# Performance work log

Hardware: AMD Instinct MI355X
Metric: run time of the kernel (lower is better)

The kernel has to match this reference:

```python
import jax, jax.numpy as jnp
import numpy as np

B, C, N = 2, 29, 8192
S, K = 1024, 16  # npoint, nsample
D = C + 3


def fps(xyz_t, npoint):
    # xyz_t: [B, N, 3] -> indices [B, npoint] (furthest point sampling, starts at idx 0)
    b, n, _ = xyz_t.shape

    def step(carry, _):
        dists, farthest = carry  # [B,N], [B]
        centroid = jnp.take_along_axis(xyz_t, farthest[:, None, None], axis=1)  # [B,1,3]
        d = jnp.sum((xyz_t - centroid) ** 2, axis=-1)  # [B,N]
        dists = jnp.minimum(dists, d)
        nxt = jnp.argmax(dists, axis=-1)
        return (dists, nxt), farthest

    init = (jnp.full((b, n), 1e10, xyz_t.dtype), jnp.zeros((b,), jnp.int32))
    _, idx = jax.lax.scan(step, init, None, length=npoint)
    return jnp.transpose(idx)  # [B, npoint]


def knn_self(pts, k):
    # pts: [B, S, 3] -> k nearest neighbor indices within the same set, [B, S, k]
    sq = jnp.sum(pts * pts, axis=-1)
    d2 = sq[:, :, None] + sq[:, None, :] - 2.0 * jnp.einsum('bic,bjc->bij', pts, pts)
    _, idx = jax.lax.top_k(-d2, k)
    return idx


def group(arr, idx):
    # arr: [B, C, N], idx: [B, S, K] -> [B, C, S, K]
    return jax.vmap(lambda a, i: a[:, i])(arr, idx)


def squeeze_2x2(x):
    # RealNVP alt-order squeeze: [n, c, h, w] -> [n, 4c, h/2, w/2]
    tl = x[:, :, 0::2, 0::2]
    br = x[:, :, 1::2, 1::2]
    tr = x[:, :, 0::2, 1::2]
    bl = x[:, :, 1::2, 0::2]
    return jnp.concatenate([tl, br, tr, bl], axis=1)


def conv2d(x, w):
    return jax.lax.conv_general_dilated(
        x, w, window_strides=(1, 1), padding='VALID',
        dimension_numbers=('NCHW', 'OIHW', 'NCHW'))


def setup_inputs() -> dict:
    key = jax.random.key(0)
    ks = jax.random.split(key, 6)
    return {
        'xyz': jax.random.normal(ks[0], (B, 3, N), jnp.float32),
        'feats': jax.random.normal(ks[1], (B, C, N), jnp.float32),
        'w0': jax.random.normal(ks[2], (64, 2 * D * 4, 3, 3), jnp.float32) * 0.02,
        'w1': jax.random.normal(ks[3], (64, 64, 3, 3), jnp.float32) * 0.02,
        'w2': jax.random.normal(ks[4], (128, 64, 3, 3), jnp.float32) * 0.02,
        'w3': jax.random.normal(ks[5], (128, 128, 2, 2), jnp.float32) * 0.02,
    }


def reference(xyz, feats, w0, w1, w2, w3):
    b, c, n = feats.shape
    xyz_t = jnp.transpose(xyz, (0, 2, 1))  # [B,N,3]
    fps_idx = fps(xyz_t, S)  # [B,S]
    new_xyz = jnp.take_along_axis(xyz, fps_idx[:, None, :], axis=2)  # [B,3,S]
    new_xyz_t = jnp.transpose(new_xyz, (0, 2, 1))  # [B,S,3]
    idx = knn_self(new_xyz_t, K)  # [B,S,K], values in [0,S)

    pos_grouped = group(new_xyz, idx)  # [B,3,S,K]
    feats_grouped = group(feats, idx)  # [B,C,S,K] (indices < S, as in original)
    pos_diff = pos_grouped - new_xyz[:, :, :, None]
    fg = jnp.concatenate([pos_diff, feats_grouped], axis=1)  # [B,D,S,K]

    # pairwise outer-product features; second half ([fg;1] x [fg;1] upper block) is all ones
    outer = jnp.einsum('bdsi,bdsj->bdsij', fg, fg)  # [B,D,S,K,K]
    mat = jnp.concatenate([outer, jnp.ones_like(outer)], axis=1)  # [B,2D,S,K,K]
    mat = jnp.transpose(mat, (0, 2, 1, 3, 4)).reshape(b * S, 2 * D, K, K)
    mat = squeeze_2x2(mat)  # [B*S, 8D, K/2, K/2]

    for w in (w0, w1, w2, w3):  # use_bn=False -> Identity bns; spatial 8->6->4->2->1
        mat = jax.nn.relu(conv2d(mat, w))

    new_points = jnp.transpose(mat.reshape(b, S, -1), (0, 2, 1))  # [B,128,S]
    return new_xyz, new_points, fps_idx
```

## Files before the change

kernel.cpp:

```cpp
#include <hip/hip_runtime.h>
#include <hip/hip_bf16.h>

#pragma clang fp contract(off)

#define NPTS 8192
#define NS   1024
#define NB   2
#define NC   29
#define NK   16


__global__ __launch_bounds__(256) void prep_kernel(
    const float* __restrict__ w0, const float* __restrict__ w1,
    const float* __restrict__ w2, const float* __restrict__ w3,
    float* __restrict__ w0t, float* __restrict__ w1t,
    float* __restrict__ w2t, float* __restrict__ w3t,
    float* __restrict__ bias0)
{
    int i = blockIdx.x * 256 + threadIdx.x;
    int n = gridDim.x * 256;
    for (int e = i; e < 73728; e += n) {
        int o = e & 63, r = e >> 6, tap = r % 9, ic2 = r / 9;
        int ic = ((ic2 >> 5) << 6) + (ic2 & 31);
        w0t[e] = w0[(o * 256 + ic) * 9 + tap];
    }
    for (int e = i; e < 36864; e += n) {
        int o = e & 63, r = e >> 6, tap = r % 9, ic = r / 9;
        w1t[e] = w1[(o * 64 + ic) * 9 + tap];
    }
    for (int e = i; e < 73728; e += n) {
        int o = e & 127, r = e >> 7, tap = r % 9, ic = r / 9;
        w2t[e] = w2[(o * 64 + ic) * 9 + tap];
    }
    for (int e = i; e < 65536; e += n) {
        int o = e & 127, r = e >> 7, tap = r & 3, ic = r >> 2;
        w3t[e] = w3[(o * 128 + ic) * 4 + tap];
    }
    if (i < 64) {
        float sum = 0.0f;
        for (int q = 0; q < 4; ++q)
            for (int c = 0; c < 32; ++c)
                for (int t = 0; t < 9; ++t)
                    sum += w0[(i * 256 + q * 64 + 32 + c) * 9 + t];
        bias0[i] = sum;
    }
}

__device__ __forceinline__ float wave_max_nonneg(float x) {
    int v = __float_as_int(x);
    int t;
    t = __builtin_amdgcn_update_dpp(0, v, 0x111, 0xf, 0xf, true);
    v = __float_as_int(fmaxf(__int_as_float(v), __int_as_float(t)));
    t = __builtin_amdgcn_update_dpp(0, v, 0x112, 0xf, 0xf, true);
    v = __float_as_int(fmaxf(__int_as_float(v), __int_as_float(t)));
    t = __builtin_amdgcn_update_dpp(0, v, 0x114, 0xf, 0xf, true);
    v = __float_as_int(fmaxf(__int_as_float(v), __int_as_float(t)));
    t = __builtin_amdgcn_update_dpp(0, v, 0x118, 0xf, 0xf, true);
    v = __float_as_int(fmaxf(__int_as_float(v), __int_as_float(t)));
    t = __builtin_amdgcn_update_dpp(0, v, 0x142, 0xa, 0xf, true);
    v = __float_as_int(fmaxf(__int_as_float(v), __int_as_float(t)));
    t = __builtin_amdgcn_update_dpp(0, v, 0x143, 0xc, 0xf, true);
    v = __float_as_int(fmaxf(__int_as_float(v), __int_as_float(t)));
    return __int_as_float(__builtin_amdgcn_readlane(v, 63));
}

__global__ __launch_bounds__(512, 2) void fps_kernel(
    const float* __restrict__ xyz,
    float* __restrict__ nx_ws, float* __restrict__ out)
{
    int b = blockIdx.x;
    int tid = threadIdx.x;
    const float* X = xyz + b * 3 * NPTS;

    __shared__ float s_xyz[3 * NPTS];
    __shared__ unsigned long long s_key[NS];

    float px[16], py[16], pz[16], dist[16];
#pragma unroll
    for (int i = 0; i < 16; ++i) {
        int gi = i * 512 + tid;
        float x = X[gi], y = X[NPTS + gi], z = X[2 * NPTS + gi];
        px[i] = x; py[i] = y; pz[i] = z;
        dist[i] = 1e10f;
        s_xyz[gi] = x; s_xyz[NPTS + gi] = y; s_xyz[2 * NPTS + gi] = z;
    }
    for (int i = tid; i < NS; i += 512) s_key[i] = 0ull;
    if (tid == 0) s_key[0] = 0xFFFFFFFFull;
    __syncthreads();

    float cx = s_xyz[0], cy = s_xyz[NPTS], cz = s_xyz[2 * NPTS];

    for (int it = 1; it < NS; ++it) {
#pragma unroll
        for (int i = 0; i < 16; ++i)
            asm volatile("" : "+v"(px[i]), "+v"(py[i]), "+v"(pz[i]));
#pragma unroll
        for (int i = 0; i < 16; ++i) {
            float dx = px[i] - cx, dy = py[i] - cy, dz = pz[i] - cz;
            float d = (dx * dx + dy * dy) + dz * dz;
            dist[i] = fminf(dist[i], d);
        }
        float t8[8];
#pragma unroll
        for (int i = 0; i < 8; ++i) t8[i] = fmaxf(dist[2 * i], dist[2 * i + 1]);
        float t4[4];
#pragma unroll
        for (int i = 0; i < 4; ++i) t4[i] = fmaxf(t8[2 * i], t8[2 * i + 1]);
        float bv = fmaxf(fmaxf(t4[0], t4[1]), fmaxf(t4[2], t4[3]));
        float wm = wave_max_nonneg(bv);
        if (bv == wm) {
            int gi = 0;
#pragma unroll
            for (int i = 15; i >= 0; --i)
                if (dist[i] == wm) gi = i * 512 + tid;
            unsigned long long key =
                ((unsigned long long)__float_as_uint(wm) << 32) | (unsigned)(~gi);
            atomicMax(&s_key[it], key);
        }
        __syncthreads();
        int idx = (int)(~(unsigned)s_key[it]);
        cx = s_xyz[idx]; cy = s_xyz[NPTS + idx]; cz = s_xyz[2 * NPTS + idx];
    }

    float* out_fps = out + 268288 + b * NS;
    for (int i = tid; i < NS; i += 512) {
        int j = (int)(~(unsigned)s_key[i]);
        out_fps[i] = (float)j;
        float x = s_xyz[j], y = s_xyz[NPTS + j], z = s_xyz[2 * NPTS + j];
        nx_ws[(b * 3 + 0) * NS + i] = x; out[(b * 3 + 0) * NS + i] = x;
        nx_ws[(b * 3 + 1) * NS + i] = y; out[(b * 3 + 1) * NS + i] = y;
        nx_ws[(b * 3 + 2) * NS + i] = z; out[(b * 3 + 2) * NS + i] = z;
    }
}

__global__ __launch_bounds__(256) void knn_kernel(
    const float* __restrict__ nx_ws, int* __restrict__ knn_ws)
{
    int q = blockIdx.x * 4 + (threadIdx.x >> 6);
    int lane = threadIdx.x & 63;
    int b = q >> 10, s = q & 1023;
    const float* P = nx_ws + b * 3 * NS;
    float qx = P[s], qy = P[NS + s], qz = P[2 * NS + s];
    float sqq = (qx * qx + qy * qy) + qz * qz;
    int base_j = lane * 16;
    float d2[16];
    {
        const float4* x4 = (const float4*)(P + base_j);
        const float4* y4 = (const float4*)(P + NS + base_j);
        const float4* z4 = (const float4*)(P + 2 * NS + base_j);
#pragma unroll
        for (int t = 0; t < 4; ++t) {
            float4 xv = x4[t], yv = y4[t], zv = z4[t];
            float xs[4] = { xv.x, xv.y, xv.z, xv.w };
            float ys[4] = { yv.x, yv.y, yv.z, yv.w };
            float zs[4] = { zv.x, zv.y, zv.z, zv.w };
#pragma unroll
            for (int e = 0; e < 4; ++e) {
                float xj = xs[e], yj = ys[e], zj = zs[e];
                float sqj = (xj * xj + yj * yj) + zj * zj;
                float dot = (qx * xj + qy * yj) + qz * zj;
                d2[t * 4 + e] = (sqq + sqj) - 2.0f * dot;
            }
        }
    }
    for (int r = 0; r < NK; ++r) {
        float lv = 3.0e38f; int li = 0;
#pragma unroll
        for (int i = 0; i < 16; ++i) { if (d2[i] < lv) { lv = d2[i]; li = i; } }
        int gj = base_j + li;
#pragma unroll
        for (int off = 32; off > 0; off >>= 1) {
            float ov = __shfl_xor(lv, off, 64);
            int   oj = __shfl_xor(gj, off, 64);
            if (ov < lv || (ov == lv && oj < gj)) { lv = ov; gj = oj; }
        }
        if (lane == 0) knn_ws[q * NK + r] = gj;
        if ((gj >> 4) == lane) {
            int li2 = gj & 15;
#pragma unroll
            for (int i = 0; i < 16; ++i) if (i == li2) d2[i] = 3.0e38f;
        }
    }
}

template<int G>
__device__ __forceinline__ void conv0_accum(
    const float* __restrict__ s_fg, const float* __restrict__ wbase, float acc[9])
{
    constexpr int r0 = G + (G >> 1);
    constexpr int GODD = G & 1;
#pragma unroll
    for (int q = 0; q < 4; ++q) {
        const int ro = q & 1, co = ((q + 1) >> 1) & 1;
        const float* wq = wbase + q * 32 * 9 * 64;
        for (int ch = 0; ch < 32; ++ch) {
            const float4* f4 = (const float4*)(s_fg + ch * 16);
            float4 v0 = f4[0], v1 = f4[1], v2 = f4[2], v3 = f4[3];
            float fg[16] = { v0.x, v0.y, v0.z, v0.w,  v1.x, v1.y, v1.z, v1.w,
                             v2.x, v2.y, v2.z, v2.w,  v3.x, v3.y, v3.z, v3.w };
            float rr[32];
#pragma unroll
            for (int j = 0; j < 4; ++j) {
                float aj = fg[2 * (r0 + j) + ro];
#pragma unroll
                for (int v = 0; v < 8; ++v)
                    rr[j * 8 + v] = aj * fg[2 * v + co];
            }
            float w[9];
#pragma unroll
            for (int t = 0; t < 9; ++t) w[t] = wq[(ch * 9 + t) * 64];
#pragma unroll
            for (int pp = 0; pp < 9; ++pp) {
                const int ly = GODD ? (pp < 3 ? 0 : 1) : (pp < 6 ? 0 : 1);
                const int xx = GODD ? (pp < 3 ? pp + 3 : pp - 3) : (pp < 6 ? pp : pp - 6);
#pragma unroll
                for (int ky = 0; ky < 3; ++ky)
#pragma unroll
                    for (int kx = 0; kx < 3; ++kx)
                        acc[pp] = __builtin_fmaf(w[ky * 3 + kx], rr[(ly + ky) * 8 + xx + kx], acc[pp]);
            }
        }
    }
}

__global__ __launch_bounds__(256, 4) void conv_kernel(
    const float* __restrict__ feats, const float* __restrict__ nx_ws,
    const int* __restrict__ knn_ws,
    const float* __restrict__ w0t, const float* __restrict__ bias0,
    const float* __restrict__ w1t, const float* __restrict__ w2t,
    const float* __restrict__ w3t, float* __restrict__ out)
{
    __shared__ float s_fg[512];
    __shared__ int   s_ni[16];
    __shared__ float s_a1[64 * 36];
    __shared__ float s_a2[64 * 16];
    __shared__ float s_a3[128 * 4];

    int bs = blockIdx.x, b = bs >> 10, s = bs & 1023;
    int tid = threadIdx.x;
    if (tid < 16) s_ni[tid] = knn_ws[bs * NK + tid];
    __syncthreads();
    const float* P = nx_ws + b * 3 * NS;
#pragma unroll
    for (int e = tid; e < 512; e += 256) {
        int d = e >> 4, k = e & 15; int j = s_ni[k];
        float v = (d < 3) ? (P[d * NS + j] - P[d * NS + s])
                          : feats[(b * NC + (d - 3)) * NPTS + j];
        s_fg[e] = v;
    }
    __syncthreads();

    int o = tid & 63, g = tid >> 6;
    {
        float acc[9];
        float bz = bias0[o];
#pragma unroll
        for (int p = 0; p < 9; ++p) acc[p] = bz;
        const float* wb = w0t + o;
        if      (g == 0) conv0_accum<0>(s_fg, wb, acc);
        else if (g == 1) conv0_accum<1>(s_fg, wb, acc);
        else if (g == 2) conv0_accum<2>(s_fg, wb, acc);
        else             conv0_accum<3>(s_fg, wb, acc);
#pragma unroll
        for (int pp = 0; pp < 9; ++pp) s_a1[o * 36 + g * 9 + pp] = fmaxf(acc[pp], 0.0f);
    }
    __syncthreads();
    {
        float a[4] = {0, 0, 0, 0};
        const float* wb = w1t + o;
        for (int ic = 0; ic < 64; ++ic) {
            const float2* ar2 = (const float2*)(s_a1 + ic * 36 + g * 6);
            float r[18];
#pragma unroll
            for (int t = 0; t < 9; ++t) { float2 tv = ar2[t]; r[t*2] = tv.x; r[t*2+1] = tv.y; }
            float w[9];
#pragma unroll
            for (int t = 0; t < 9; ++t) w[t] = wb[(ic * 9 + t) * 64];
#pragma unroll
            for (int x = 0; x < 4; ++x)
#pragma unroll
                for (int ky = 0; ky < 3; ++ky)
#pragma unroll
                    for (int kx = 0; kx < 3; ++kx)
                        a[x] = __builtin_fmaf(w[ky * 3 + kx], r[ky * 6 + x + kx], a[x]);
        }
#pragma unroll
        for (int x = 0; x < 4; ++x) s_a2[o * 16 + g * 4 + x] = fmaxf(a[x], 0.0f);
    }
    __syncthreads();
    {
        int o2 = tid & 127, g2 = tid >> 7;
        float a[2] = {0, 0};
        const float* wb = w2t + o2;
        for (int ic = 0; ic < 64; ++ic) {
            const float4* ar4 = (const float4*)(s_a2 + ic * 16 + g2 * 4);
            float r[12];
#pragma unroll
            for (int t = 0; t < 3; ++t) { float4 tv = ar4[t]; r[t*4]=tv.x; r[t*4+1]=tv.y; r[t*4+2]=tv.z; r[t*4+3]=tv.w; }
            float w[9];
#pragma unroll
            for (int t = 0; t < 9; ++t) w[t] = wb[(ic * 9 + t) * 128];
#pragma unroll
            for (int x = 0; x < 2; ++x)
#pragma unroll
                for (int ky = 0; ky < 3; ++ky)
#pragma unroll
                    for (int kx = 0; kx < 3; ++kx)
                        a[x] = __builtin_fmaf(w[ky * 3 + kx], r[ky * 4 + x + kx], a[x]);
        }
#pragma unroll
        for (int x = 0; x < 2; ++x) s_a3[o2 * 4 + g2 * 2 + x] = fmaxf(a[x], 0.0f);
    }
    __syncthreads();
    if (tid < 128) {
        float acc = 0.0f;
        const float* wb = w3t + tid;
        for (int ic = 0; ic < 128; ++ic) {
            float4 av = *(const float4*)(s_a3 + ic * 4);
            float wa = wb[(ic * 4 + 0) * 128];
            float wbv = wb[(ic * 4 + 1) * 128];
            float wc = wb[(ic * 4 + 2) * 128];
            float wd = wb[(ic * 4 + 3) * 128];
            acc = __builtin_fmaf(wa, av.x, acc);
            acc = __builtin_fmaf(wbv, av.y, acc);
            acc = __builtin_fmaf(wc, av.z, acc);
            acc = __builtin_fmaf(wd, av.w, acc);
        }
        out[6144 + (b * 128 + tid) * NS + s] = fmaxf(acc, 0.0f);
    }
}

extern "C" void kernel_launch(void* const* d_in, const int* in_sizes, int n_in,
                              void* d_out, int out_size, void* d_ws, size_t ws_size,
                              hipStream_t stream) {
    const float* xyz   = (const float*)d_in[0];
    const float* feats = (const float*)d_in[1];
    const float* w0    = (const float*)d_in[2];
    const float* w1    = (const float*)d_in[3];
    const float* w2    = (const float*)d_in[4];
    const float* w3    = (const float*)d_in[5];
    float* out = (float*)d_out;

    char* ws = (char*)d_ws;
    float* nx_ws  = (float*)(ws + 8192);
    int*   knn_ws = (int*)(ws + 32768);
    float* w0t    = (float*)(ws + 163840);
    float* bias0  = (float*)(ws + 458752);
    float* w1t    = (float*)(ws + 459008);
    float* w2t    = (float*)(ws + 606464);
    float* w3t    = (float*)(ws + 901376);

    prep_kernel<<<128, 256, 0, stream>>>(w0, w1, w2, w3, w0t, w1t, w2t, w3t, bias0);
    fps_kernel<<<NB, 512, 0, stream>>>(xyz, nx_ws, out);
    knn_kernel<<<(NB * NS) / 4, 256, 0, stream>>>(nx_ws, knn_ws);
    conv_kernel<<<NB * NS, 256, 0, stream>>>(feats, nx_ws, knn_ws, w0t, bias0, w1t, w2t, w3t, out);
}
```

Before: 1.431 ms.

## Stage conv0 and conv1 weights through double-buffered shared memory

Conv0 and conv1 now load their weights from global memory cooperatively, four input channels at a time, into a double-buffered shared-memory tile. The next chunk is prefetched into registers while the current chunk is consumed. Previously each of the four thread groups fetched the same weights from global memory on its own. This aims to cut redundant global/L1 traffic and hide load latency, at the cost of about 18KB more LDS per block and a barrier per chunk, including barriers inside branches that differ per group.

```diff
diff --git a/kernel.cpp b/kernel.cpp
--- a/kernel.cpp
+++ b/kernel.cpp
@@ -184,41 +184,69 @@
 }
 
 template<int G>
-__device__ __forceinline__ void conv0_accum(
-    const float* __restrict__ s_fg, const float* __restrict__ wbase, float acc[9])
+__device__ __forceinline__ void conv0_staged(
+    const float* __restrict__ s_fg, float* __restrict__ s_w,
+    const float* __restrict__ w0t, int o, float acc[9])
 {
     constexpr int r0 = G + (G >> 1);
     constexpr int GODD = G & 1;
+    {
+        float st[9];
+#pragma unroll
+        for (int j = 0; j < 9; ++j) st[j] = w0t[(G * 9 + j) * 64 + o];
+#pragma unroll
+        for (int j = 0; j < 9; ++j) s_w[(G * 9 + j) * 64 + o] = st[j];
+    }
+    __syncthreads();
+    int buf = 0;
 #pragma unroll
     for (int q = 0; q < 4; ++q) {
         const int ro = q & 1, co = ((q + 1) >> 1) & 1;
-        const float* wq = wbase + q * 32 * 9 * 64;
-        for (int ch = 0; ch < 32; ++ch) {
-            const float4* f4 = (const float4*)(s_fg + ch * 16);
-            float4 v0 = f4[0], v1 = f4[1], v2 = f4[2], v3 = f4[3];
-            float fg[16] = { v0.x, v0.y, v0.z, v0.w,  v1.x, v1.y, v1.z, v1.w,
-                             v2.x, v2.y, v2.z, v2.w,  v3.x, v3.y, v3.z, v3.w };
-            float rr[32];
-#pragma unroll
-            for (int j = 0; j < 4; ++j) {
-                float aj = fg[2 * (r0 + j) + ro];
-#pragma unroll
-                for (int v = 0; v < 8; ++v)
-                    rr[j * 8 + v] = aj * fg[2 * v + co];
-            }
-            float w[9];
-#pragma unroll
-            for (int t = 0; t < 9; ++t) w[t] = wq[(ch * 9 + t) * 64];
-#pragma unroll
-            for (int pp = 0; pp < 9; ++pp) {
-                const int ly = GODD ? (pp < 3 ? 0 : 1) : (pp < 6 ? 0 : 1);
-                const int xx = GODD ? (pp < 3 ? pp + 3 : pp - 3) : (pp < 6 ? pp : pp - 6);
-#pragma unroll
-                for (int ky = 0; ky < 3; ++ky)
-#pragma unroll
-                    for (int kx = 0; kx < 3; ++kx)
-                        acc[pp] = __builtin_fmaf(w[ky * 3 + kx], rr[(ly + ky) * 8 + xx + kx], acc[pp]);
-            }
+        for (int cc = 0; cc < 8; ++cc) {
+            int K = q * 8 + cc;
+            float st[9];
+            if (K < 31) {
+                const float* gsrc = w0t + (K + 1) * 36 * 64;
+#pragma unroll
+                for (int j = 0; j < 9; ++j) st[j] = gsrc[(G * 9 + j) * 64 + o];
+            }
+            const float* wl = s_w + buf * 2304;
+#pragma unroll
+            for (int chl = 0; chl < 4; ++chl) {
+                int ch = cc * 4 + chl;
+                const float4* f4 = (const float4*)(s_fg + ch * 16);
+                float4 v0 = f4[0], v1 = f4[1], v2 = f4[2], v3 = f4[3];
+                float fg[16] = { v0.x, v0.y, v0.z, v0.w,  v1.x, v1.y, v1.z, v1.w,
+                                 v2.x, v2.y, v2.z, v2.w,  v3.x, v3.y, v3.z, v3.w };
+                float rr[32];
+#pragma unroll
+                for (int j = 0; j < 4; ++j) {
+                    float aj = fg[2 * (r0 + j) + ro];
+#pragma unroll
+                    for (int v = 0; v < 8; ++v)
+                        rr[j * 8 + v] = aj * fg[2 * v + co];
+                }
+                float w[9];
+#pragma unroll
+                for (int t = 0; t < 9; ++t) w[t] = wl[(chl * 9 + t) * 64 + o];
+#pragma unroll
+                for (int pp = 0; pp < 9; ++pp) {
+                    const int ly = GODD ? (pp < 3 ? 0 : 1) : (pp < 6 ? 0 : 1);
+                    const int xx = GODD ? (pp < 3 ? pp + 3 : pp - 3) : (pp < 6 ? pp : pp - 6);
+#pragma unroll
+                    for (int ky = 0; ky < 3; ++ky)
+#pragma unroll
+                        for (int kx = 0; kx < 3; ++kx)
+                            acc[pp] = __builtin_fmaf(w[ky * 3 + kx], rr[(ly + ky) * 8 + xx + kx], acc[pp]);
+                }
+            }
+            if (K < 31) {
+                float* wn = s_w + (buf ^ 1) * 2304;
+#pragma unroll
+                for (int j = 0; j < 9; ++j) wn[(G * 9 + j) * 64 + o] = st[j];
+            }
+            __syncthreads();
+            buf ^= 1;
         }
     }
 }
@@ -232,6 +260,7 @@
 {
     __shared__ float s_fg[512];
     __shared__ int   s_ni[16];
+    __shared__ float s_w[2 * 36 * 64];
     __shared__ float s_a1[64 * 36];
     __shared__ float s_a2[64 * 16];
     __shared__ float s_a3[128 * 4];
@@ -256,33 +285,57 @@
         float bz = bias0[o];
 #pragma unroll
         for (int p = 0; p < 9; ++p) acc[p] = bz;
-        const float* wb = w0t + o;
-        if      (g == 0) conv0_accum<0>(s_fg, wb, acc);
-        else if (g == 1) conv0_accum<1>(s_fg, wb, acc);
-        else if (g == 2) conv0_accum<2>(s_fg, wb, acc);
-        else             conv0_accum<3>(s_fg, wb, acc);
+        if      (g == 0) conv0_staged<0>(s_fg, s_w, w0t, o, acc);
+        else if (g == 1) conv0_staged<1>(s_fg, s_w, w0t, o, acc);
+        else if (g == 2) conv0_staged<2>(s_fg, s_w, w0t, o, acc);
+        else             conv0_staged<3>(s_fg, s_w, w0t, o, acc);
 #pragma unroll
         for (int pp = 0; pp < 9; ++pp) s_a1[o * 36 + g * 9 + pp] = fmaxf(acc[pp], 0.0f);
     }
+    {
+        float st[9];
+#pragma unroll
+        for (int j = 0; j < 9; ++j) st[j] = w1t[(g * 9 + j) * 64 + o];
+#pragma unroll
+        for (int j = 0; j < 9; ++j) s_w[(g * 9 + j) * 64 + o] = st[j];
+    }
     __syncthreads();
     {
         float a[4] = {0, 0, 0, 0};
-        const float* wb = w1t + o;
-        for (int ic = 0; ic < 64; ++ic) {
-            const float2* ar2 = (const float2*)(s_a1 + ic * 36 + g * 6);
-            float r[18];
-#pragma unroll
-            for (int t = 0; t < 9; ++t) { float2 tv = ar2[t]; r[t*2] = tv.x; r[t*2+1] = tv.y; }
-            float w[9];
-#pragma unroll
-            for (int t = 0; t < 9; ++t) w[t] = wb[(ic * 9 + t) * 64];
-#pragma unroll
-            for (int x = 0; x < 4; ++x)
-#pragma unroll
-                for (int ky = 0; ky < 3; ++ky)
-#pragma unroll
-                    for (int kx = 0; kx < 3; ++kx)
-                        a[x] = __builtin_fmaf(w[ky * 3 + kx], r[ky * 6 + x + kx], a[x]);
+        int buf = 0;
+        for (int c = 0; c < 16; ++c) {
+            float st[9];
+            if (c < 15) {
+                const float* gsrc = w1t + (c + 1) * 36 * 64;
+#pragma unroll
+                for (int j = 0; j < 9; ++j) st[j] = gsrc[(g * 9 + j) * 64 + o];
+            }
+            const float* wl = s_w + buf * 2304;
+#pragma unroll
+            for (int icl = 0; icl < 4; ++icl) {
+                int ic = c * 4 + icl;
+                const float2* ar2 = (const float2*)(s_a1 + ic * 36 + g * 6);
+                float r[18];
+#pragma unroll
+                for (int t = 0; t < 9; ++t) { float2 tv = ar2[t]; r[t*2] = tv.x; r[t*2+1] = tv.y; }
+                float w[9];
+#pragma unroll
+                for (int t = 0; t < 9; ++t) w[t] = wl[(icl * 9 + t) * 64 + o];
+#pragma unroll
+                for (int x = 0; x < 4; ++x)
+#pragma unroll
+                    for (int ky = 0; ky < 3; ++ky)
+#pragma unroll
+                        for (int kx = 0; kx < 3; ++kx)
+                            a[x] = __builtin_fmaf(w[ky * 3 + kx], r[ky * 6 + x + kx], a[x]);
+            }
+            if (c < 15) {
+                float* wn = s_w + (buf ^ 1) * 2304;
+#pragma unroll
+                for (int j = 0; j < 9; ++j) wn[(g * 9 + j) * 64 + o] = st[j];
+            }
+            __syncthreads();
+            buf ^= 1;
         }
 #pragma unroll
         for (int x = 0; x < 4; ++x) s_a2[o * 16 + g * 4 + x] = fmaxf(a[x], 0.0f);
```

Result: slower. 1.461 ms (+2.1%).
